# Optimization experiments

Measured on AMD Instinct MI355X. Metric: run time of the kernel, lower is better.

## Reference

```python
import jax, jax.numpy as jnp
import numpy as np

EPS = 1e-8
NUM_LAYERS = 6


def setup_inputs() -> dict:
    key = jax.random.key(0)
    ks = jax.random.split(key, 8)
    N, Cin, Cout, S, H, W = 4, 256, 256, 512, 64, 64
    fan_in = Cin  # kaiming for 1x1 conv, leaky_relu a=0 -> gain sqrt(2)
    return {
        "x": jax.random.normal(ks[0], (N, Cin, H, W), dtype=jnp.float32),
        "y": jax.random.normal(ks[1], (N, S), dtype=jnp.float32),
        "ch_conv_w": jax.random.normal(ks[2], (Cout, Cin), dtype=jnp.float32) / np.sqrt(fan_in),
        "ch_conv_b": jnp.zeros((Cout,), dtype=jnp.float32),
        "affine_w": jax.random.normal(ks[3], (NUM_LAYERS, Cout, S), dtype=jnp.float32) / np.sqrt(S),
        "affine_b": jnp.zeros((NUM_LAYERS, Cout), dtype=jnp.float32),
        "mod_w": jax.random.normal(ks[4], (NUM_LAYERS, Cout, Cout), dtype=jnp.float32) * np.sqrt(2.0 / Cout),
    }


def _forward(x, y, ch_conv_w, ch_conv_b, affine_w, affine_b, mod_w):
    # 1x1 channel conv (with bias)
    x = jnp.einsum("oi,bihw->bohw", ch_conv_w, x) + ch_conv_b[None, :, None, None]
    x = jnp.repeat(jnp.repeat(x, 2, axis=2), 2, axis=3)
    # channel repeat_interleave(2) -> [N, 2C, H, W]
    x = jnp.repeat(x, 2, axis=1)

    C = x.shape[1] // 2
    for i in range(NUM_LAYERS):
        x1, x2 = x[:, :C], x[:, C:]
        # SpatialShift2d with default directions pads [1,1,1,1] (replicate) then
        # crops the identical region for every split -> exact identity.
        y1 = x1 + x2
        # g-branch: Conv2dMod(k=1) with per-sample style modulation + exact GELU
        s = jnp.einsum("cs,bs->bc", affine_w[i], y) + affine_b[i]  # [B, C]
        wmod = mod_w[i][None] * (s[:, :, None] + 1.0)              # [B, O, I] (style scales OUTPUT channel)
        d = jax.lax.rsqrt(jnp.sum(wmod * wmod, axis=2, keepdims=True) + EPS)
        wmod = wmod * d
        h = jnp.einsum("boi,bihw->bohw", wmod, y1)
        y2 = x2 + jax.nn.gelu(h, approximate=False)
        x = jnp.concatenate([y1, y2], axis=1)

    x1, x2 = x[:, :C], x[:, C:]
    return (x1 + x2) * 0.5


def reference(x, y, ch_conv_w, ch_conv_b, affine_w, affine_b, mod_w):
    return _forward(x, y, ch_conv_w, ch_conv_b, affine_w, affine_b, mod_w)
```

## Files before the change

### kernel.cpp

```cpp
#include <hip/hip_runtime.h>
#include <math.h>

#define NB 4
#define CC 256
#define SS 512
#define NL 6
#define SLOT_HW 65536
#define G_OFF_HW   (7*SLOT_HW)

typedef __attribute__((ext_vector_type(8))) short s16x8;
typedef __attribute__((ext_vector_type(4))) float f32x4;
typedef __attribute__((ext_vector_type(2))) float f32x2;

__device__ __forceinline__ unsigned short f2bf(float f) {
    unsigned u = __builtin_bit_cast(unsigned, f);
    u += 0x7FFFu + ((u >> 16) & 1u);
    return (unsigned short)(u >> 16);
}
__device__ __forceinline__ unsigned cvt_pk_bf16(float lo, float hi) {
    unsigned r;
    asm("v_cvt_pk_bf16_f32 %0, %1, %2" : "=v"(r) : "v"(lo), "v"(hi));
    return r;
}
__device__ __forceinline__ float gelu_fast(float x) {
    float u = x * (1.0f + 0.044715f * x * x);
    float e = __expf(-1.5957691216f * u);
    return x * __builtin_amdgcn_rcpf(1.0f + e);
}
__device__ __forceinline__ s16x8 aload(const unsigned short* p) {
    s16x8 r;
    asm volatile("global_load_dwordx4 %0, %1, off" : "=v"(r) : "v"(p));
    return r;
}

__global__ __launch_bounds__(256) void prep_kernel(
    const float* __restrict__ y, const float* __restrict__ aw,
    const float* __restrict__ ab, const float* __restrict__ mw,
    const float* __restrict__ cw, unsigned short* __restrict__ wsBF)
{
    int w = threadIdx.x >> 6, lane = threadIdx.x & 63;
    float* gtab = (float*)(wsBF + G_OFF_HW);

    if (blockIdx.x < 448) {
        int row = blockIdx.x*4 + w;
        int sl  = row >> 8, m = row & 255;
        const float* src = (sl == 0) ? (cw + (size_t)m*CC)
                                     : (mw + ((size_t)(sl-1)*CC + m)*CC);
        unsigned short* dst = wsBF + (size_t)sl*SLOT_HW;
#pragma unroll
        for (int u = 0; u < 4; ++u) {
            int k = lane + 64*u;
            int f = (m >> 4)*8 + (k >> 5);
            int hw = f*512 + ((k >> 3) & 3)*128 + (m & 15)*8 + (k & 7);
            dst[hw] = f2bf(src[k]);
        }
        return;
    }

    int r  = (blockIdx.x - 448)*4 + w;
    int pl = r >> 8, po = r & 255;

    const float* awr = aw + (size_t)(pl*CC + po)*SS;
    float s[4] = {0.f, 0.f, 0.f, 0.f};
#pragma unroll
    for (int j = 0; j < 8; ++j) {
        int idx = lane + 64*j;
        float a = awr[idx];
#pragma unroll
        for (int b = 0; b < 4; ++b) s[b] += a * y[(size_t)b*SS + idx];
    }
    const float* mwr = mw + ((size_t)pl*CC + po)*CC;
    float qs = 0.f;
#pragma unroll
    for (int u = 0; u < 4; ++u) { float v = mwr[lane + 64*u]; qs += v*v; }
#pragma unroll
    for (int off = 32; off; off >>= 1) {
#pragma unroll
        for (int b = 0; b < 4; ++b) s[b] += __shfl_xor(s[b], off);
        qs += __shfl_xor(qs, off);
    }
    float abv = ab[pl*CC + po];
    if (lane < 4) {
        float t = s[lane] + abv + 1.0f;
        gtab[pl*1024 + lane*256 + po] = t * (1.0f / sqrtf(t*t*qs + 1e-8f));
    }
}

#define BFRAGL(buf, kq, nt, kcl) \
    (lds + (buf)*16384 + ((((kq)*2 + (nt))*2 + (kcl)))*1024)

#define ISSUE(p) { \
    aS[p][0] = aload(slot + (size_t)(((2*w+0)*8 + (p))*512) + lane*8); \
    aS[p][1] = aload(slot + (size_t)(((2*w+1)*8 + (p))*512) + lane*8); }
#define WAITA(N, st) asm volatile("s_waitcnt vmcnt(" #N ")" \
    : "+v"(aS[st][0]), "+v"(aS[st][1]))
#define STEPX(st) { \
    s16x8 b0 = *(const s16x8*)(BFRAGL(buf,(st)>>1,0,(st)&1) + lane*16); \
    s16x8 b1 = *(const s16x8*)(BFRAGL(buf,(st)>>1,1,(st)&1) + lane*16); \
    acc[0][0] = __builtin_amdgcn_mfma_f32_16x16x32_bf16(aS[st][0], b0, acc[0][0],0,0,0); \
    acc[1][0] = __builtin_amdgcn_mfma_f32_16x16x32_bf16(aS[st][1], b0, acc[1][0],0,0,0); \
    acc[0][1] = __builtin_amdgcn_mfma_f32_16x16x32_bf16(aS[st][0], b1, acc[0][1],0,0,0); \
    acc[1][1] = __builtin_amdgcn_mfma_f32_16x16x32_bf16(aS[st][1], b1, acc[1][1],0,0,0); \
}
#define MFMA_PHASE() \
    ISSUE(5); WAITA(10,0); STEPX(0); \
    ISSUE(6); WAITA(10,1); STEPX(1); \
    ISSUE(7); WAITA(10,2); STEPX(2); \
    WAITA(8,3);  STEPX(3); \
    WAITA(6,4);  STEPX(4); \
    WAITA(4,5);  STEPX(5); \
    WAITA(2,6);  STEPX(6); \
    WAITA(0,7);  STEPX(7);
#define RAW_BARRIER() { \
    asm volatile("s_waitcnt lgkmcnt(0)" ::: "memory"); \
    __builtin_amdgcn_s_barrier(); }

__global__ __launch_bounds__(512, 4) void fused_kernel(
    const float* __restrict__ x, const float* __restrict__ cb,
    const unsigned short* __restrict__ wsBF, float* __restrict__ out)
{
    __shared__ __align__(16) unsigned char lds[75776];
    float* xS = (float*)(lds + 32768);
    float* S2 = (float*)(lds + 32768);
    float* gS = (float*)(lds + 69632);
    const float* gtab = (const float*)(wsBF + G_OFF_HW);

    const int tid  = threadIdx.x;
    const int lane = tid & 63;
    const int w    = tid >> 6;
    const int l15  = lane & 15;
    const int q    = lane >> 4;

    const int bswz  = blockIdx.x & 7;
    const int b     = bswz >> 1;
    const int half  = bswz & 1;
    const int strip = blockIdx.x >> 3;
    const int n0    = strip * 64 + half * 32;

    float y1[2][2][4], y2[2][2][4];
    f32x4 acc[2][2];
    s16x8 aS[8][2];

#pragma unroll
    for (int t = 0; t < 2; ++t)
#pragma unroll
        for (int s = 0; s < 2; ++s) acc[t][s] = 0;

    if (tid < 384) {
        int gl = tid >> 6, gm = (tid & 63) * 4;
        float4 gvv = *(const float4*)&gtab[gl*1024 + b*256 + gm];
        *(float4*)&gS[gl*256 + gm] = gvv;
    }
#pragma unroll
    for (int p = 0; p < 4; ++p) {
        int row = (tid >> 3) + 64*p, c4 = (tid & 7) * 4;
        float4 v = *(const float4*)&x[((size_t)(b*CC + row))*4096 + n0 + c4];
        *(float4*)&xS[row*36 + c4] = v;
    }
    asm volatile("" ::: "memory");
    {
        const unsigned short* slot = wsBF;
#pragma unroll
        for (int p = 0; p < 5; ++p) ISSUE(p);
        RAW_BARRIER();
        {
            int n = tid & 31, k0 = (tid >> 5) * 16;
            int nt = n >> 4, n15 = n & 15;
#pragma unroll
            for (int j = 0; j < 4; ++j) {
                int k = k0 + 4*j;
                float v0 = xS[(k+0)*36 + n], v1 = xS[(k+1)*36 + n];
                float v2 = xS[(k+2)*36 + n], v3 = xS[(k+3)*36 + n];
                uint2 hv; hv.x = cvt_pk_bf16(v0, v1); hv.y = cvt_pk_bf16(v2, v3);
                int kq = k >> 6, kcl = (k >> 5) & 1, qq = (k >> 3) & 3, jb = k & 7;
                *(uint2*)(BFRAGL(0,kq,nt,kcl) + (16*qq + n15)*16 + jb*2) = hv;
            }
        }
        RAW_BARRIER();
        const int buf = 0;
        __builtin_amdgcn_s_setprio(1);
        MFMA_PHASE();
        __builtin_amdgcn_s_setprio(0);
    }

#pragma unroll
    for (int t = 0; t < 2; ++t)
#pragma unroll
    for (int s = 0; s < 2; ++s)
#pragma unroll
    for (int r = 0; r < 4; ++r) {
        int m  = 32*w + 16*t + 4*q + r;
        int nl = 16*s + l15;
        S2[m*33 + nl] = acc[t][s][r] + cb[m];
    }
    __syncthreads();
#pragma unroll
    for (int t = 0; t < 2; ++t)
#pragma unroll
    for (int s = 0; s < 2; ++s)
#pragma unroll
    for (int r = 0; r < 4; ++r) {
        int c  = 32*w + 16*t + 4*q + r;
        int nl = 16*s + l15;
        float a  = S2[(c >> 1)*33 + nl];
        float bb = S2[(128 + (c >> 1))*33 + nl];
        y1[t][s][r] = a + bb;
        y2[t][s][r] = bb;
    }

    for (int l = 0; l < NL; ++l) {
        const int buf = l & 1;
        const unsigned short* slot = wsBF + (size_t)(1 + l)*SLOT_HW;
#pragma unroll
        for (int t = 0; t < 2; ++t)
#pragma unroll
            for (int s = 0; s < 2; ++s) acc[t][s] = 0;

        asm volatile("" ::: "memory");
#pragma unroll
        for (int p = 0; p < 5; ++p) ISSUE(p);

        {
            int kq = w >> 1, kcl = w & 1, jb = 4*(q & 1);
#pragma unroll
            for (int t = 0; t < 2; ++t) {
                int qq = 2*t + (q >> 1);
#pragma unroll
                for (int s = 0; s < 2; ++s) {
                    uint2 hv;
                    hv.x = cvt_pk_bf16(y1[t][s][0], y1[t][s][1]);
                    hv.y = cvt_pk_bf16(y1[t][s][2], y1[t][s][3]);
                    *(uint2*)(BFRAGL(buf,kq,s,kcl) + (16*qq + l15)*16 + jb*2) = hv;
                }
            }
        }
        RAW_BARRIER();
        __builtin_amdgcn_s_setprio(1);
        MFMA_PHASE();
        __builtin_amdgcn_s_setprio(0);

        float4 gv[2];
#pragma unroll
        for (int t = 0; t < 2; ++t)
            gv[t] = *(const float4*)&gS[l*256 + 32*w + 16*t + 4*q];

        if (l < NL - 1) {
#pragma unroll
            for (int t = 0; t < 2; ++t)
#pragma unroll
            for (int s = 0; s < 2; ++s)
#pragma unroll
            for (int r = 0; r < 4; ++r) {
                y2[t][s][r] += gelu_fast(acc[t][s][r] * gv[t][r]);
                y1[t][s][r] += y2[t][s][r];
            }
        } else {
#pragma unroll
            for (int t = 0; t < 2; ++t)
#pragma unroll
            for (int s = 0; s < 2; ++s)
#pragma unroll
            for (int r = 0; r < 4; ++r) {
                float yf = y2[t][s][r] + gelu_fast(acc[t][s][r] * gv[t][r]);
                float v  = 0.5f*(y1[t][s][r] + yf);
                int ch  = 32*w + 16*t + 4*q + r;
                int wpx = half*32 + 16*s + l15;
                f32x2 vv = {v, v};
                size_t base = (((size_t)(b*CC + ch)*128 + 2*strip))*128 + 2*wpx;
                __builtin_nontemporal_store(vv, (f32x2*)&out[base]);
                __builtin_nontemporal_store(vv, (f32x2*)&out[base + 128]);
            }
        }
    }
}

extern "C" void kernel_launch(void* const* d_in, const int* in_sizes, int n_in,
                              void* d_out, int out_size, void* d_ws, size_t ws_size,
                              hipStream_t stream) {
    const float* x  = (const float*)d_in[0];
    const float* y  = (const float*)d_in[1];
    const float* cw = (const float*)d_in[2];
    const float* cb = (const float*)d_in[3];
    const float* aw = (const float*)d_in[4];
    const float* ab = (const float*)d_in[5];
    const float* mw = (const float*)d_in[6];
    float* out = (float*)d_out;

    unsigned short* wsBF = (unsigned short*)d_ws;

    prep_kernel<<<832, 256, 0, stream>>>(y, aw, ab, mw, cw, wsBF);
    fused_kernel<<<512, 512, 0, stream>>>(x, cb, wsBF, out);
}
```

Baseline: 119.6 us.

## Prefetch next layer's weights across epilogue and software-pipeline LDS B-fragment reads

All eight A-operand weight loads for the next layer are now issued right after the current layer's MFMA phase, so the global-load latency overlaps the GELU epilogue and LDS staging instead of sitting at the top of the next layer. The MFMA phase double-buffers the B-fragment LDS reads, loading step k+1 while step k's MFMAs run, and the s_setprio bracketing is removed. In exchange more A registers stay live across the epilogue, which raises register pressure and may hurt occupancy at 512 threads with 4 blocks per CU.

Measured after the change: 132.3 us. 1.11x slower.

```diff
diff --git a/kernel.cpp b/kernel.cpp
--- a/kernel.cpp
+++ b/kernel.cpp
@@ -92,25 +92,26 @@
 #define ISSUE(p) { \
     aS[p][0] = aload(slot + (size_t)(((2*w+0)*8 + (p))*512) + lane*8); \
     aS[p][1] = aload(slot + (size_t)(((2*w+1)*8 + (p))*512) + lane*8); }
+#define ISSUE_ALL() { ISSUE(0); ISSUE(1); ISSUE(2); ISSUE(3); \
+                      ISSUE(4); ISSUE(5); ISSUE(6); ISSUE(7); }
 #define WAITA(N, st) asm volatile("s_waitcnt vmcnt(" #N ")" \
     : "+v"(aS[st][0]), "+v"(aS[st][1]))
-#define STEPX(st) { \
-    s16x8 b0 = *(const s16x8*)(BFRAGL(buf,(st)>>1,0,(st)&1) + lane*16); \
-    s16x8 b1 = *(const s16x8*)(BFRAGL(buf,(st)>>1,1,(st)&1) + lane*16); \
-    acc[0][0] = __builtin_amdgcn_mfma_f32_16x16x32_bf16(aS[st][0], b0, acc[0][0],0,0,0); \
-    acc[1][0] = __builtin_amdgcn_mfma_f32_16x16x32_bf16(aS[st][1], b0, acc[1][0],0,0,0); \
-    acc[0][1] = __builtin_amdgcn_mfma_f32_16x16x32_bf16(aS[st][0], b1, acc[0][1],0,0,0); \
-    acc[1][1] = __builtin_amdgcn_mfma_f32_16x16x32_bf16(aS[st][1], b1, acc[1][1],0,0,0); \
-}
-#define MFMA_PHASE() \
-    ISSUE(5); WAITA(10,0); STEPX(0); \
-    ISSUE(6); WAITA(10,1); STEPX(1); \
-    ISSUE(7); WAITA(10,2); STEPX(2); \
-    WAITA(8,3);  STEPX(3); \
-    WAITA(6,4);  STEPX(4); \
-    WAITA(4,5);  STEPX(5); \
-    WAITA(2,6);  STEPX(6); \
-    WAITA(0,7);  STEPX(7);
+#define BRD(st, nt) (*(const s16x8*)(BFRAGL(buf,(st)>>1,(nt),(st)&1) + lane*16))
+#define MM(st, bv0, bv1) { \
+    acc[0][0] = __builtin_amdgcn_mfma_f32_16x16x32_bf16(aS[st][0], bv0, acc[0][0],0,0,0); \
+    acc[1][0] = __builtin_amdgcn_mfma_f32_16x16x32_bf16(aS[st][1], bv0, acc[1][0],0,0,0); \
+    acc[0][1] = __builtin_amdgcn_mfma_f32_16x16x32_bf16(aS[st][0], bv1, acc[0][1],0,0,0); \
+    acc[1][1] = __builtin_amdgcn_mfma_f32_16x16x32_bf16(aS[st][1], bv1, acc[1][1],0,0,0); }
+#define MFMA_PHASE() { \
+    s16x8 cb0 = BRD(0,0), cb1 = BRD(0,1), nb0, nb1; \
+    WAITA(14,0); nb0 = BRD(1,0); nb1 = BRD(1,1); MM(0,cb0,cb1); \
+    WAITA(12,1); cb0 = BRD(2,0); cb1 = BRD(2,1); MM(1,nb0,nb1); \
+    WAITA(10,2); nb0 = BRD(3,0); nb1 = BRD(3,1); MM(2,cb0,cb1); \
+    WAITA(8,3);  cb0 = BRD(4,0); cb1 = BRD(4,1); MM(3,nb0,nb1); \
+    WAITA(6,4);  nb0 = BRD(5,0); nb1 = BRD(5,1); MM(4,cb0,cb1); \
+    WAITA(4,5);  cb0 = BRD(6,0); cb1 = BRD(6,1); MM(5,nb0,nb1); \
+    WAITA(2,6);  nb0 = BRD(7,0); nb1 = BRD(7,1); MM(6,cb0,cb1); \
+    WAITA(0,7);  MM(7,nb0,nb1); }
 #define RAW_BARRIER() { \
     asm volatile("s_waitcnt lgkmcnt(0)" ::: "memory"); \
     __builtin_amdgcn_s_barrier(); }
@@ -160,8 +161,7 @@
     asm volatile("" ::: "memory");
     {
         const unsigned short* slot = wsBF;
-#pragma unroll
-        for (int p = 0; p < 5; ++p) ISSUE(p);
+        ISSUE_ALL();
         RAW_BARRIER();
         {
             int n = tid & 31, k0 = (tid >> 5) * 16;
@@ -178,9 +178,7 @@
         }
         RAW_BARRIER();
         const int buf = 0;
-        __builtin_amdgcn_s_setprio(1);
         MFMA_PHASE();
-        __builtin_amdgcn_s_setprio(0);
     }
 
 #pragma unroll
@@ -208,17 +206,18 @@
         y2[t][s][r] = bb;
     }
 
+    const unsigned short* slotp = wsBF + SLOT_HW;
+    {
+        const unsigned short* slot = slotp;
+        asm volatile("" ::: "memory");
+        ISSUE_ALL();
+    }
     for (int l = 0; l < NL; ++l) {
         const int buf = l & 1;
-        const unsigned short* slot = wsBF + (size_t)(1 + l)*SLOT_HW;
 #pragma unroll
         for (int t = 0; t < 2; ++t)
 #pragma unroll
             for (int s = 0; s < 2; ++s) acc[t][s] = 0;
-
-        asm volatile("" ::: "memory");
-#pragma unroll
-        for (int p = 0; p < 5; ++p) ISSUE(p);
 
         {
             int kq = w >> 1, kcl = w & 1, jb = 4*(q & 1);
@@ -235,9 +234,14 @@
             }
         }
         RAW_BARRIER();
-        __builtin_amdgcn_s_setprio(1);
         MFMA_PHASE();
-        __builtin_amdgcn_s_setprio(0);
+
+        if (l + 1 < NL) {
+            slotp += SLOT_HW;
+            const unsigned short* slot = slotp;
+            asm volatile("" ::: "memory");
+            ISSUE_ALL();
+        }
 
         float4 gv[2];
 #pragma unroll
```
